# Kernel tuning notes

Measured on AMD Instinct MI355X. Metric: run time of the kernel, lower is better.

The kernel has to match this reference:

```python
import jax, jax.numpy as jnp
import numpy as np

VOCAB, EMB_DIM, HIDDEN, NUM_CLASSES = 50000, 300, 1000, 5
B, MAX_LEN = 4096, 128


def setup_inputs() -> dict:
    key = jax.random.key(0)
    k1, k2, k3, k4, k5, k6, k7 = jax.random.split(key, 7)
    x = jax.random.randint(k1, (B, MAX_LEN), 0, VOCAB, dtype=jnp.int64)
    lengths = jnp.maximum(jax.random.randint(k2, (B,), 0, MAX_LEN, dtype=jnp.int64), 1)
    emb_table = jax.random.normal(k3, (VOCAB, EMB_DIM), dtype=jnp.float32) * 0.1
    W1 = jax.random.normal(k4, (2 * EMB_DIM, HIDDEN), dtype=jnp.float32) * (1.0 / np.sqrt(2 * EMB_DIM))
    b1 = jax.random.normal(k5, (HIDDEN,), dtype=jnp.float32) * 0.01
    W2 = jax.random.normal(k6, (HIDDEN, NUM_CLASSES), dtype=jnp.float32) * (1.0 / np.sqrt(HIDDEN))
    b2 = jax.random.normal(k7, (NUM_CLASSES,), dtype=jnp.float32) * 0.01
    return {"x": x, "lengths": lengths, "emb_table": emb_table,
            "W1": W1, "b1": b1, "W2": W2, "b2": b2}


def reference(x, lengths, emb_table, W1, b1, W2, b2):
    emb = emb_table[x]                                  # [B, L, D] gather
    mask = (jnp.arange(emb.shape[1])[None, :] < lengths[:, None])  # [B, L]
    m = mask[:, :, None].astype(emb.dtype)
    avg_pool = jnp.sum(emb * m, axis=1) / lengths[:, None].astype(emb.dtype)  # [B, D]
    neg_inf = jnp.finfo(emb.dtype).min
    max_pool = jnp.max(jnp.where(mask[:, :, None], emb, neg_inf), axis=1)     # [B, D]
    rep = jnp.concatenate([avg_pool, max_pool], axis=1)  # [B, 2D]
    hidden = jax.nn.relu(rep @ W1 + b1)                  # [B, 1000]
    logits = hidden @ W2 + b2                            # [B, C]
    return logits
```

## Files before the change

kernel.cpp:

```cpp
#include <hip/hip_runtime.h>
#include <float.h>
#include <stdint.h>

#define EMB_DIM  300
#define MAX_LEN  128
#define HIDDEN   1000
#define NCLS     5
#define VOCAB_SZ 50000
#define KPAD     640
#define NPAD     1024

typedef float    f32x4  __attribute__((ext_vector_type(4)));
typedef __bf16   bf16x8 __attribute__((ext_vector_type(8)));
typedef unsigned short ushort8v __attribute__((ext_vector_type(8)));

__device__ __forceinline__ unsigned short f2bf(float f) {
    union { float f; uint32_t u; } v; v.f = f;
    uint32_t u = v.u;
    return (unsigned short)((u + 0x7FFFu + ((u >> 16) & 1u)) >> 16);
}
__device__ __forceinline__ float bf2f(unsigned short h) {
    union { uint32_t u; float f; } v; v.u = ((uint32_t)h) << 16;
    return v.f;
}

__global__ __launch_bounds__(256) void transpose_w1(
    const float* __restrict__ W1, unsigned short* __restrict__ Bt)
{
    __shared__ float t[32][33];
    const int tx = threadIdx.x & 31, ty = threadIdx.x >> 5;
    const int n0 = blockIdx.x * 32, k0 = blockIdx.y * 32;
    #pragma unroll
    for (int i = 0; i < 4; ++i) {
        int k = k0 + ty + i * 8, n = n0 + tx;
        t[ty + i * 8][tx] = (k < 600 && n < HIDDEN) ? W1[(size_t)k * HIDDEN + n] : 0.f;
    }
    __syncthreads();
    #pragma unroll
    for (int i = 0; i < 4; ++i) {
        int n = n0 + ty + i * 8, k = k0 + tx;
        Bt[(size_t)n * KPAD + k] = f2bf(t[tx][ty + i * 8]);
    }
}

__global__ __launch_bounds__(128) void pool_kernel(
    const int* __restrict__ x, const int* __restrict__ lengths,
    const float* __restrict__ emb, unsigned short* __restrict__ rep)
{
    const int b = blockIdx.x;
    const int t = threadIdx.x;

    __shared__ int sidx[MAX_LEN];
    sidx[t] = x[b * MAX_LEN + t];
    __syncthreads();

    unsigned short* rb = rep + (size_t)b * KPAD;

    if (t >= 75) {
        if (t < 85) {
            ushort4 z = {0, 0, 0, 0};
            *(ushort4*)(rb + 600 + (t - 75) * 4) = z;
        }
        return;
    }

    int L = lengths[b];
    L = max(1, min(L, MAX_LEN));

    const int d = t * 4;
    float4 s  = {0.f, 0.f, 0.f, 0.f};
    float4 mx = {-FLT_MAX, -FLT_MAX, -FLT_MAX, -FLT_MAX};

    for (int i = 0; i < L; ++i) {
        int idx = sidx[i];
        idx = max(0, min(idx, VOCAB_SZ - 1));
        const float4 v = *(const float4*)(emb + (size_t)idx * EMB_DIM + d);
        s.x += v.x; s.y += v.y; s.z += v.z; s.w += v.w;
        mx.x = fmaxf(mx.x, v.x); mx.y = fmaxf(mx.y, v.y);
        mx.z = fmaxf(mx.z, v.z); mx.w = fmaxf(mx.w, v.w);
    }

    const float inv = 1.0f / (float)L;
    ushort4 av, mv;
    av.x = f2bf(s.x * inv); av.y = f2bf(s.y * inv);
    av.z = f2bf(s.z * inv); av.w = f2bf(s.w * inv);
    mv.x = f2bf(mx.x); mv.y = f2bf(mx.y); mv.z = f2bf(mx.z); mv.w = f2bf(mx.w);
    *(ushort4*)(rb + d)       = av;
    *(ushort4*)(rb + 300 + d) = mv;
}

#define BM 128
#define BN 64
#define BK 32

__global__ __launch_bounds__(256, 2) void gemm1_mfma(
    const unsigned short* __restrict__ A,
    const unsigned short* __restrict__ Bt,
    const float* __restrict__ bias,
    unsigned short* __restrict__ H,
    int M)
{
    __shared__ unsigned short As[2][BM * BK];
    __shared__ unsigned short Bs[2][BN * BK];

    const int tid  = threadIdx.x;
    const int wv   = tid >> 6;
    const int lane = tid & 63;
    const int bm   = blockIdx.y * BM;
    const int bn   = blockIdx.x * BN;
    const int wr   = (wv & 1) * 64;
    const int wc   = (wv >> 1) * 32;

    f32x4 acc[4][2] = {};

    auto stage = [&](int buf, int k0) {
        #pragma unroll
        for (int j = 0; j < 2; ++j) {
            int ci  = (wv * 2 + j) * 64 + lane;
            int row = ci >> 2, c = ci & 3;
            const unsigned short* g = A + (size_t)(bm + row) * KPAD + k0 + c * 8;
            unsigned short* l = &As[buf][(wv * 2 + j) * 512];
            __builtin_amdgcn_global_load_lds(g, l, 16, 0, 0);
        }
        {
            int ci  = wv * 64 + lane;
            int row = ci >> 2, c = ci & 3;
            const unsigned short* g = Bt + (size_t)(bn + row) * KPAD + k0 + c * 8;
            unsigned short* l = &Bs[buf][wv * 512];
            __builtin_amdgcn_global_load_lds(g, l, 16, 0, 0);
        }
    };

    stage(0, 0);
    int cur = 0;
    const int q = lane >> 4, r16 = lane & 15;

    for (int it = 0; it < KPAD / BK; ++it) {
        __syncthreads();
        if (it + 1 < KPAD / BK) stage(cur ^ 1, (it + 1) * BK);

        bf16x8 af[4], bfr[2];
        #pragma unroll
        for (int mi = 0; mi < 4; ++mi) {
            int row = wr + mi * 16 + r16;
            af[mi] = *(const bf16x8*)&As[cur][row * BK + q * 8];
        }
        #pragma unroll
        for (int nj = 0; nj < 2; ++nj) {
            int row = wc + nj * 16 + r16;
            bfr[nj] = *(const bf16x8*)&Bs[cur][row * BK + q * 8];
        }
        #pragma unroll
        for (int mi = 0; mi < 4; ++mi)
            #pragma unroll
            for (int nj = 0; nj < 2; ++nj)
                acc[mi][nj] = __builtin_amdgcn_mfma_f32_16x16x32_bf16(
                    af[mi], bfr[nj], acc[mi][nj], 0, 0, 0);
        cur ^= 1;
    }

    #pragma unroll
    for (int nj = 0; nj < 2; ++nj) {
        int n = bn + wc + nj * 16 + r16;
        if (n >= HIDDEN) continue;
        float bv = bias[n];
        #pragma unroll
        for (int mi = 0; mi < 4; ++mi) {
            #pragma unroll
            for (int r = 0; r < 4; ++r) {
                int m = bm + wr + mi * 16 + q * 4 + r;
                float v = acc[mi][nj][r] + bv;
                H[(size_t)m * HIDDEN + n] = f2bf(fmaxf(v, 0.f));
            }
        }
    }
}

__global__ __launch_bounds__(64) void gemm2_kernel(
    const unsigned short* __restrict__ Hb,
    const float* __restrict__ W2,
    const float* __restrict__ b2,
    float* __restrict__ out)
{
    const int b = blockIdx.x, lane = threadIdx.x;
    const unsigned short* hr = Hb + (size_t)b * HIDDEN;

    float acc[NCLS] = {0.f, 0.f, 0.f, 0.f, 0.f};
    #pragma unroll
    for (int c = 0; c < 2; ++c) {
        int k0 = c * 512 + lane * 8;
        if (k0 < HIDDEN) {
            ushort8v hv = *(const ushort8v*)(hr + k0);
            #pragma unroll
            for (int j = 0; j < 8; ++j) {
                float h = bf2f(hv[j]);
                const float* w = W2 + (size_t)(k0 + j) * NCLS;
                #pragma unroll
                for (int cc = 0; cc < NCLS; ++cc) acc[cc] += h * w[cc];
            }
        }
    }
    #pragma unroll
    for (int off = 32; off > 0; off >>= 1)
        #pragma unroll
        for (int cc = 0; cc < NCLS; ++cc)
            acc[cc] += __shfl_down(acc[cc], off, 64);

    if (lane == 0) {
        #pragma unroll
        for (int cc = 0; cc < NCLS; ++cc)
            out[(size_t)b * NCLS + cc] = acc[cc] + b2[cc];
    }
}

extern "C" void kernel_launch(void* const* d_in, const int* in_sizes, int n_in,
                              void* d_out, int out_size, void* d_ws, size_t ws_size,
                              hipStream_t stream)
{
    const int*   x       = (const int*)d_in[0];
    const int*   lengths = (const int*)d_in[1];
    const float* emb     = (const float*)d_in[2];
    const float* W1      = (const float*)d_in[3];
    const float* b1      = (const float*)d_in[4];
    const float* W2      = (const float*)d_in[5];
    const float* b2      = (const float*)d_in[6];
    float*       out     = (float*)d_out;

    const int B = in_sizes[1];

    unsigned short* rep    = (unsigned short*)d_ws;
    unsigned short* w1t    = rep + (size_t)B * KPAD;
    unsigned short* hidden = w1t + (size_t)NPAD * KPAD;

    transpose_w1<<<dim3(32, 20), 256, 0, stream>>>(W1, w1t);
    pool_kernel<<<B, 128, 0, stream>>>(x, lengths, emb, rep);

    dim3 g1(NPAD / BN, B / BM);
    gemm1_mfma<<<g1, 256, 0, stream>>>(rep, w1t, b1, hidden, B);

    gemm2_kernel<<<B, 64, 0, stream>>>(hidden, W2, b2, out);
}
```

Baseline: 168.4 us.

## Fuse second GEMM into first GEMM epilogue and split pooling over four token groups

The hidden activations are no longer written to memory. Instead the first GEMM's epilogue applies bias and ReLU, multiplies by W2 in registers, reduces across lanes with shuffles and atomically adds partial logits into an output that a new init kernel pre-fills with b2. The pooling kernel now uses 300 threads, with four token groups striding the sequence and two loads in flight per iteration, then combines partial sum and max through shared memory. This removes the hidden-buffer round trip and one kernel launch and adds memory-level parallelism to the gather. The cost is many atomics (16 column-blocks per row) and a nondeterministic summation order.

New measurement: 226.8 us. +34.7%, slower.

```diff
diff --git a/kernel.cpp b/kernel.cpp
--- a/kernel.cpp
+++ b/kernel.cpp
@@ -12,16 +12,18 @@
 
 typedef float    f32x4  __attribute__((ext_vector_type(4)));
 typedef __bf16   bf16x8 __attribute__((ext_vector_type(8)));
-typedef unsigned short ushort8v __attribute__((ext_vector_type(8)));
 
 __device__ __forceinline__ unsigned short f2bf(float f) {
     union { float f; uint32_t u; } v; v.f = f;
     uint32_t u = v.u;
     return (unsigned short)((u + 0x7FFFu + ((u >> 16) & 1u)) >> 16);
 }
-__device__ __forceinline__ float bf2f(unsigned short h) {
-    union { uint32_t u; float f; } v; v.u = ((uint32_t)h) << 16;
-    return v.f;
+
+__global__ __launch_bounds__(256) void init_out(
+    float* __restrict__ out, const float* __restrict__ b2, int n)
+{
+    int i = blockIdx.x * 256 + threadIdx.x;
+    if (i < n) out[i] = b2[i % NCLS];
 }
 
 __global__ __launch_bounds__(256) void transpose_w1(
@@ -43,61 +45,92 @@
     }
 }
 
-__global__ __launch_bounds__(128) void pool_kernel(
+__global__ __launch_bounds__(300) void pool_kernel(
     const int* __restrict__ x, const int* __restrict__ lengths,
     const float* __restrict__ emb, unsigned short* __restrict__ rep)
 {
-    const int b = blockIdx.x;
-    const int t = threadIdx.x;
-
-    __shared__ int sidx[MAX_LEN];
-    sidx[t] = x[b * MAX_LEN + t];
+    const int b  = blockIdx.x;
+    const int tx = threadIdx.x;
+    const int ty = threadIdx.y;
+
+    __shared__ int   sidx[MAX_LEN];
+    __shared__ float psum[3][EMB_DIM];
+    __shared__ float pmax[3][EMB_DIM];
+
+    const int lin = ty * 75 + tx;
+    if (lin < MAX_LEN) sidx[lin] = x[b * MAX_LEN + lin];
     __syncthreads();
-
-    unsigned short* rb = rep + (size_t)b * KPAD;
-
-    if (t >= 75) {
-        if (t < 85) {
-            ushort4 z = {0, 0, 0, 0};
-            *(ushort4*)(rb + 600 + (t - 75) * 4) = z;
-        }
-        return;
-    }
 
     int L = lengths[b];
     L = max(1, min(L, MAX_LEN));
 
-    const int d = t * 4;
+    const int d = tx * 4;
     float4 s  = {0.f, 0.f, 0.f, 0.f};
     float4 mx = {-FLT_MAX, -FLT_MAX, -FLT_MAX, -FLT_MAX};
 
-    for (int i = 0; i < L; ++i) {
-        int idx = sidx[i];
-        idx = max(0, min(idx, VOCAB_SZ - 1));
-        const float4 v = *(const float4*)(emb + (size_t)idx * EMB_DIM + d);
-        s.x += v.x; s.y += v.y; s.z += v.z; s.w += v.w;
-        mx.x = fmaxf(mx.x, v.x); mx.y = fmaxf(mx.y, v.y);
-        mx.z = fmaxf(mx.z, v.z); mx.w = fmaxf(mx.w, v.w);
-    }
-
-    const float inv = 1.0f / (float)L;
-    ushort4 av, mv;
-    av.x = f2bf(s.x * inv); av.y = f2bf(s.y * inv);
-    av.z = f2bf(s.z * inv); av.w = f2bf(s.w * inv);
-    mv.x = f2bf(mx.x); mv.y = f2bf(mx.y); mv.z = f2bf(mx.z); mv.w = f2bf(mx.w);
-    *(ushort4*)(rb + d)       = av;
-    *(ushort4*)(rb + 300 + d) = mv;
+    int i = ty;
+    for (; i + 4 < L; i += 8) {
+        int i0 = max(0, min(sidx[i],     VOCAB_SZ - 1));
+        int i1 = max(0, min(sidx[i + 4], VOCAB_SZ - 1));
+        const float4 v0 = *(const float4*)(emb + (size_t)i0 * EMB_DIM + d);
+        const float4 v1 = *(const float4*)(emb + (size_t)i1 * EMB_DIM + d);
+        s.x += v0.x; s.y += v0.y; s.z += v0.z; s.w += v0.w;
+        mx.x = fmaxf(mx.x, v0.x); mx.y = fmaxf(mx.y, v0.y);
+        mx.z = fmaxf(mx.z, v0.z); mx.w = fmaxf(mx.w, v0.w);
+        s.x += v1.x; s.y += v1.y; s.z += v1.z; s.w += v1.w;
+        mx.x = fmaxf(mx.x, v1.x); mx.y = fmaxf(mx.y, v1.y);
+        mx.z = fmaxf(mx.z, v1.z); mx.w = fmaxf(mx.w, v1.w);
+    }
+    if (i < L) {
+        int i0 = max(0, min(sidx[i], VOCAB_SZ - 1));
+        const float4 v0 = *(const float4*)(emb + (size_t)i0 * EMB_DIM + d);
+        s.x += v0.x; s.y += v0.y; s.z += v0.z; s.w += v0.w;
+        mx.x = fmaxf(mx.x, v0.x); mx.y = fmaxf(mx.y, v0.y);
+        mx.z = fmaxf(mx.z, v0.z); mx.w = fmaxf(mx.w, v0.w);
+    }
+
+    if (ty > 0) {
+        *(float4*)&psum[ty - 1][d] = s;
+        *(float4*)&pmax[ty - 1][d] = mx;
+    }
+    __syncthreads();
+
+    unsigned short* rb = rep + (size_t)b * KPAD;
+
+    if (ty == 0) {
+        #pragma unroll
+        for (int g = 0; g < 3; ++g) {
+            float4 ps = *(const float4*)&psum[g][d];
+            float4 pm = *(const float4*)&pmax[g][d];
+            s.x += ps.x; s.y += ps.y; s.z += ps.z; s.w += ps.w;
+            mx.x = fmaxf(mx.x, pm.x); mx.y = fmaxf(mx.y, pm.y);
+            mx.z = fmaxf(mx.z, pm.z); mx.w = fmaxf(mx.w, pm.w);
+        }
+        const float inv = 1.0f / (float)L;
+        ushort4 av, mv;
+        av.x = f2bf(s.x * inv); av.y = f2bf(s.y * inv);
+        av.z = f2bf(s.z * inv); av.w = f2bf(s.w * inv);
+        mv.x = f2bf(mx.x); mv.y = f2bf(mx.y);
+        mv.z = f2bf(mx.z); mv.w = f2bf(mx.w);
+        *(ushort4*)(rb + d)       = av;
+        *(ushort4*)(rb + 300 + d) = mv;
+    }
+    if (ty == 1 && tx < 10) {
+        ushort4 z = {0, 0, 0, 0};
+        *(ushort4*)(rb + 600 + tx * 4) = z;
+    }
 }
 
 #define BM 128
 #define BN 64
 #define BK 32
 
-__global__ __launch_bounds__(256, 2) void gemm1_mfma(
+__global__ __launch_bounds__(256, 2) void gemm1_fused(
     const unsigned short* __restrict__ A,
     const unsigned short* __restrict__ Bt,
     const float* __restrict__ bias,
-    unsigned short* __restrict__ H,
+    const float* __restrict__ W2,
+    float* __restrict__ out,
     int M)
 {
     __shared__ unsigned short As[2][BM * BK];
@@ -141,15 +174,11 @@
 
         bf16x8 af[4], bfr[2];
         #pragma unroll
-        for (int mi = 0; mi < 4; ++mi) {
-            int row = wr + mi * 16 + r16;
-            af[mi] = *(const bf16x8*)&As[cur][row * BK + q * 8];
-        }
-        #pragma unroll
-        for (int nj = 0; nj < 2; ++nj) {
-            int row = wc + nj * 16 + r16;
-            bfr[nj] = *(const bf16x8*)&Bs[cur][row * BK + q * 8];
-        }
+        for (int mi = 0; mi < 4; ++mi)
+            af[mi] = *(const bf16x8*)&As[cur][(wr + mi * 16 + r16) * BK + q * 8];
+        #pragma unroll
+        for (int nj = 0; nj < 2; ++nj)
+            bfr[nj] = *(const bf16x8*)&Bs[cur][(wc + nj * 16 + r16) * BK + q * 8];
         #pragma unroll
         for (int mi = 0; mi < 4; ++mi)
             #pragma unroll
@@ -159,57 +188,45 @@
         cur ^= 1;
     }
 
+    float bv[2];
+    float w2v[2][NCLS];
     #pragma unroll
     for (int nj = 0; nj < 2; ++nj) {
         int n = bn + wc + nj * 16 + r16;
-        if (n >= HIDDEN) continue;
-        float bv = bias[n];
-        #pragma unroll
-        for (int mi = 0; mi < 4; ++mi) {
-            #pragma unroll
-            for (int r = 0; r < 4; ++r) {
+        if (n < HIDDEN) {
+            bv[nj] = bias[n];
+            #pragma unroll
+            for (int c = 0; c < NCLS; ++c) w2v[nj][c] = W2[(size_t)n * NCLS + c];
+        } else {
+            bv[nj] = 0.f;
+            #pragma unroll
+            for (int c = 0; c < NCLS; ++c) w2v[nj][c] = 0.f;
+        }
+    }
+
+    #pragma unroll
+    for (int mi = 0; mi < 4; ++mi) {
+        #pragma unroll
+        for (int r = 0; r < 4; ++r) {
+            float p[NCLS] = {0.f, 0.f, 0.f, 0.f, 0.f};
+            #pragma unroll
+            for (int nj = 0; nj < 2; ++nj) {
+                float h = fmaxf(acc[mi][nj][r] + bv[nj], 0.f);
+                #pragma unroll
+                for (int c = 0; c < NCLS; ++c) p[c] += h * w2v[nj][c];
+            }
+            #pragma unroll
+            for (int off = 1; off < 16; off <<= 1)
+                #pragma unroll
+                for (int c = 0; c < NCLS; ++c)
+                    p[c] += __shfl_xor(p[c], off, 64);
+            if (r16 == 0) {
                 int m = bm + wr + mi * 16 + q * 4 + r;
-                float v = acc[mi][nj][r] + bv;
-                H[(size_t)m * HIDDEN + n] = f2bf(fmaxf(v, 0.f));
+                #pragma unroll
+                for (int c = 0; c < NCLS; ++c)
+                    atomicAdd(&out[(size_t)m * NCLS + c], p[c]);
             }
         }
-    }
-}
-
-__global__ __launch_bounds__(64) void gemm2_kernel(
-    const unsigned short* __restrict__ Hb,
-    const float* __restrict__ W2,
-    const float* __restrict__ b2,
-    float* __restrict__ out)
-{
-    const int b = blockIdx.x, lane = threadIdx.x;
-    const unsigned short* hr = Hb + (size_t)b * HIDDEN;
-
-    float acc[NCLS] = {0.f, 0.f, 0.f, 0.f, 0.f};
-    #pragma unroll
-    for (int c = 0; c < 2; ++c) {
-        int k0 = c * 512 + lane * 8;
-        if (k0 < HIDDEN) {
-            ushort8v hv = *(const ushort8v*)(hr + k0);
-            #pragma unroll
-            for (int j = 0; j < 8; ++j) {
-                float h = bf2f(hv[j]);
-                const float* w = W2 + (size_t)(k0 + j) * NCLS;
-                #pragma unroll
-                for (int cc = 0; cc < NCLS; ++cc) acc[cc] += h * w[cc];
-            }
-        }
-    }
-    #pragma unroll
-    for (int off = 32; off > 0; off >>= 1)
-        #pragma unroll
-        for (int cc = 0; cc < NCLS; ++cc)
-            acc[cc] += __shfl_down(acc[cc], off, 64);
-
-    if (lane == 0) {
-        #pragma unroll
-        for (int cc = 0; cc < NCLS; ++cc)
-            out[(size_t)b * NCLS + cc] = acc[cc] + b2[cc];
     }
 }
 
@@ -228,15 +245,13 @@
 
     const int B = in_sizes[1];
 
-    unsigned short* rep    = (unsigned short*)d_ws;
-    unsigned short* w1t    = rep + (size_t)B * KPAD;
-    unsigned short* hidden = w1t + (size_t)NPAD * KPAD;
-
+    unsigned short* rep = (unsigned short*)d_ws;
+    unsigned short* w1t = rep + (size_t)B * KPAD;
+
+    init_out<<<(B * NCLS + 255) / 256, 256, 0, stream>>>(out, b2, B * NCLS);
     transpose_w1<<<dim3(32, 20), 256, 0, stream>>>(W1, w1t);
-    pool_kernel<<<B, 128, 0, stream>>>(x, lengths, emb, rep);
+    pool_kernel<<<B, dim3(75, 4), 0, stream>>>(x, lengths, emb, rep);
 
     dim3 g1(NPAD / BN, B / BM);
-    gemm1_mfma<<<g1, 256, 0, stream>>>(rep, w1t, b1, hidden, B);
-
-    gemm2_kernel<<<B, 64, 0, stream>>>(hidden, W2, b2, out);
-}
+    gemm1_fused<<<g1, 256, 0, stream>>>(rep, w1t, b1, W2, out, B);
+}
```
